# Kernel optimization log

Hardware: AMD Instinct MI355X
Metric: run time of the kernel (lower is better)

## Reference

```python
import jax, jax.numpy as jnp
import numpy as np

WS = 7          # window size
NH = 12         # attention heads
D_STATE = 64    # mamba d_state
HEADDIM = 64    # mamba headdim


def layernorm(x, w, b):
    mu = jnp.mean(x, axis=-1, keepdims=True)
    var = jnp.mean((x - mu) ** 2, axis=-1, keepdims=True)
    return (x - mu) * jax.lax.rsqrt(var + 1e-5) * w + b


def mamba2(x, W_in, conv_w, conv_b, dt_bias, A_log, D, mnorm_w, W_out):
    # Mamba2 (SSD) forward: in_proj -> causal depthwise conv+silu -> selective scan -> gated RMSNorm -> out_proj
    B, L, dm = x.shape
    nheads = dt_bias.shape[0]
    d_inner = nheads * HEADDIM
    zxbcdt = x @ W_in                                   # (B,L,2*d_inner+2*d_state+nheads)
    z = zxbcdt[..., :d_inner]
    xBC = zxbcdt[..., d_inner:2 * d_inner + 2 * D_STATE]
    dt = zxbcdt[..., -nheads:]
    conv_dim = xBC.shape[-1]
    pad = conv_w.shape[-1] - 1
    xBC_t = jnp.swapaxes(xBC, 1, 2)                     # (B, conv_dim, L)
    conv_out = jax.lax.conv_general_dilated(
        xBC_t, conv_w[:, None, :], window_strides=(1,), padding=[(pad, 0)],
        feature_group_count=conv_dim, dimension_numbers=('NCH', 'OIH', 'NCH'))
    xBC = jax.nn.silu(jnp.swapaxes(conv_out, 1, 2) + conv_b)
    xs = xBC[..., :d_inner]
    Bm = xBC[..., d_inner:d_inner + D_STATE]            # (B,L,n)
    Cm = xBC[..., d_inner + D_STATE:]                   # (B,L,n)
    dt = jax.nn.softplus(dt + dt_bias)                  # (B,L,h)
    A = -jnp.exp(A_log)                                 # (h,)
    dA = jnp.exp(dt * A)                                # (B,L,h)
    xh = xs.reshape(B, L, nheads, HEADDIM)              # (B,L,h,p)

    def step(h, inp):
        dA_t, dt_t, x_t, B_t, C_t = inp                 # (B,h),(B,h),(B,h,p),(B,n),(B,n)
        dBx = (dt_t[..., None] * x_t)[..., None] * B_t[:, None, None, :]
        h = h * dA_t[..., None, None] + dBx             # (B,h,p,n)
        y = jnp.einsum('bhpn,bn->bhp', h, C_t)
        return h, y

    sw = lambda a: jnp.swapaxes(a, 0, 1)                # time-major
    h0 = jnp.zeros((B, nheads, HEADDIM, D_STATE), x.dtype)
    _, ys = jax.lax.scan(step, h0, (sw(dA), sw(dt), sw(xh), sw(Bm), sw(Cm)))
    y = jnp.swapaxes(ys, 0, 1) + D[None, None, :, None] * xh   # (B,L,h,p)
    y = y.reshape(B, L, d_inner)
    g = y * jax.nn.silu(z)                              # gated RMSNorm (norm_before_gate=False)
    g = g * jax.lax.rsqrt(jnp.mean(g * g, axis=-1, keepdims=True) + 1e-5) * mnorm_w
    return g @ W_out


def gated_window_attention(xw, qkv_w, qkv_b, gate_w, gate_b, proj_w, proj_b):
    B_, N, C = xw.shape
    hd = C // NH
    qkv = (xw @ qkv_w + qkv_b).reshape(B_, N, 3, NH, hd).transpose(2, 0, 3, 1, 4)
    q, k, v = qkv[0] * (hd ** -0.5), qkv[1], qkv[2]     # (B_,h,N,d)
    attn = jax.nn.softmax(jnp.einsum('bhnd,bhmd->bhnm', q, k), axis=-1)
    xa = jnp.einsum('bhnm,bhmd->bhnd', attn, v).transpose(0, 2, 1, 3)  # (B_,N,h,d)
    gate = jax.nn.sigmoid(xw @ gate_w + gate_b)[..., None]             # (B_,N,h,1)
    xa = (xa * gate).reshape(B_, N, C)
    return xa @ proj_w + proj_b


def lgs_forward(x, norm1_w, norm1_b, W_in, conv_w, conv_b, dt_bias, A_log, D, mnorm_w, W_out,
                qkv_w, qkv_b, gate_w, gate_b, proj_w, proj_b, fusion_w, fusion_b,
                norm2_w, norm2_b, fc1_w, fc1_b, fc2_w, fc2_b, H, W):
    B, L, C = x.shape
    shortcut = x
    xn = layernorm(x, norm1_w, norm1_b)
    # Branch A: Mamba2 global scan
    x_mamba = mamba2(xn, W_in, conv_w, conv_b, dt_bias, A_log, D, mnorm_w, W_out)
    # Branch B: gated window attention (shift_size=0 -> no roll, no mask)
    x2d = xn.reshape(B, H, W, C)
    xw = x2d.reshape(B, H // WS, WS, W // WS, WS, C).transpose(0, 1, 3, 2, 4, 5).reshape(-1, WS * WS, C)
    aw = gated_window_attention(xw, qkv_w, qkv_b, gate_w, gate_b, proj_w, proj_b)
    x_attn = aw.reshape(B, H // WS, W // WS, WS, WS, C).transpose(0, 1, 3, 2, 4, 5).reshape(B, L, C)
    # Fuse branches with 1x1 conv (== linear on channel dim)
    x_cat = jnp.concatenate([x_mamba, x_attn], axis=-1)   # (B,L,2C)
    x_fused = x_cat @ fusion_w + fusion_b
    x = shortcut + x_fused
    xn2 = layernorm(x, norm2_w, norm2_b)
    mlp = jax.nn.gelu(xn2 @ fc1_w + fc1_b, approximate=False) @ fc2_w + fc2_b
    return x + mlp


def setup_inputs() -> dict:
    key = jax.random.key(0)
    ks = jax.random.split(key, 16)
    B, H, W, C = 8, 56, 56, 384
    L = H * W
    d_inner, d_state, nheads_m, d_conv = 768, 64, 12, 4
    d_in_proj = 2 * d_inner + 2 * d_state + nheads_m   # 1676
    conv_dim = d_inner + 2 * d_state                   # 896
    s = 0.02
    return {
        'x': jax.random.normal(ks[0], (B, L, C), jnp.float32),
        'norm1_w': jnp.ones((C,), jnp.float32),
        'norm1_b': jnp.zeros((C,), jnp.float32),
        'W_in': jax.random.normal(ks[1], (C, d_in_proj), jnp.float32) * s,
        'conv_w': jax.random.normal(ks[2], (conv_dim, d_conv), jnp.float32) * 0.1,
        'conv_b': jnp.zeros((conv_dim,), jnp.float32),
        'dt_bias': jax.random.normal(ks[3], (nheads_m,), jnp.float32) * 0.5,
        'A_log': jnp.log(jax.random.uniform(ks[4], (nheads_m,), jnp.float32, 1.0, 16.0)),
        'D': jnp.ones((nheads_m,), jnp.float32),
        'mnorm_w': jnp.ones((d_inner,), jnp.float32),
        'W_out': jax.random.normal(ks[5], (d_inner, C), jnp.float32) * s,
        'qkv_w': jax.random.normal(ks[6], (C, 3 * C), jnp.float32) * s,
        'qkv_b': jnp.zeros((3 * C,), jnp.float32),
        'gate_w': jax.random.normal(ks[7], (C, NH), jnp.float32) * s,
        'gate_b': jnp.zeros((NH,), jnp.float32),
        'proj_w': jax.random.normal(ks[8], (C, C), jnp.float32) * s,
        'proj_b': jnp.zeros((C,), jnp.float32),
        'fusion_w': jax.random.normal(ks[9], (2 * C, C), jnp.float32) * s,
        'fusion_b': jnp.zeros((C,), jnp.float32),
        'norm2_w': jnp.ones((C,), jnp.float32),
        'norm2_b': jnp.zeros((C,), jnp.float32),
        'fc1_w': jax.random.normal(ks[10], (C, 4 * C), jnp.float32) * s,
        'fc1_b': jnp.zeros((4 * C,), jnp.float32),
        'fc2_w': jax.random.normal(ks[11], (4 * C, C), jnp.float32) * s,
        'fc2_b': jnp.zeros((C,), jnp.float32),
        'H': H,
        'W': W,
    }


def reference(x, norm1_w, norm1_b, W_in, conv_w, conv_b, dt_bias, A_log, D, mnorm_w, W_out,
              qkv_w, qkv_b, gate_w, gate_b, proj_w, proj_b, fusion_w, fusion_b,
              norm2_w, norm2_b, fc1_w, fc1_b, fc2_w, fc2_b, H, W):
    return lgs_forward(x, norm1_w, norm1_b, W_in, conv_w, conv_b, dt_bias, A_log, D, mnorm_w, W_out,
                       qkv_w, qkv_b, gate_w, gate_b, proj_w, proj_b, fusion_w, fusion_b,
                       norm2_w, norm2_b, fc1_w, fc1_b, fc2_w, fc2_b, H, W)
```

## Files before the change

kernel.cpp:

```cpp
#include <hip/hip_runtime.h>
#include <math.h>

static constexpr int L_SEQ  = 3136;
static constexpr int NBATCH = 8;
static constexpr int CDIM   = 384;
static constexpr int DIN    = 768;
static constexpr int NHM    = 12;
static constexpr int HDM    = 64;
static constexpr int DPROJ  = 1676;
static constexpr int CONVD  = 896;
static constexpr int NROWS  = NBATCH * L_SEQ;
static constexpr int NHA    = 12;
static constexpr int NCH    = 49;
static constexpr int CHT    = 64;
static constexpr int CTK    = 28;

typedef __attribute__((ext_vector_type(8))) short short8;
typedef __attribute__((ext_vector_type(8))) unsigned short ushort8;
typedef __attribute__((ext_vector_type(4))) float f32x4;
typedef const unsigned int __attribute__((address_space(1)))* gua_t;
typedef unsigned int __attribute__((address_space(3)))* lua_t;

__device__ __forceinline__ float siluf(float x) { return x / (1.f + __expf(-x)); }
__device__ __forceinline__ unsigned short f2bf(float f) {
  unsigned int u = __float_as_uint(f);
  u += 0x7fff + ((u >> 16) & 1);
  return (unsigned short)(u >> 16);
}
__device__ __forceinline__ float bf2f(unsigned short h) {
  return __uint_as_float(((unsigned int)h) << 16);
}
__device__ __forceinline__ float fast_erff(float x) {
  float ax = fabsf(x);
  float tt = 1.f / (1.f + 0.3275911f * ax);
  float y = tt * (0.254829592f + tt * (-0.284496736f + tt * (1.421413741f +
            tt * (-1.453152027f + tt * 1.061405429f))));
  float r = 1.f - y * __expf(-ax * ax);
  return copysignf(r, x);
}

__global__ __launch_bounds__(256) void ln_kernel(const float* __restrict__ in,
    const float* __restrict__ w, const float* __restrict__ b, unsigned short* __restrict__ out) {
  int wave = threadIdx.x >> 6, lane = threadIdx.x & 63;
  int row = blockIdx.x * 4 + wave;
  if (row >= NROWS) return;
  const float* r = in + (size_t)row * CDIM;
  float2 v[3];
  float s1 = 0.f, s2 = 0.f;
#pragma unroll
  for (int q = 0; q < 3; q++) {
    v[q] = *(const float2*)&r[q * 128 + lane * 2];
    s1 += v[q].x + v[q].y;
    s2 += v[q].x * v[q].x + v[q].y * v[q].y;
  }
#pragma unroll
  for (int o = 32; o > 0; o >>= 1) { s1 += __shfl_xor(s1, o, 64); s2 += __shfl_xor(s2, o, 64); }
  float mu = s1 * (1.f / 384.f);
  float var = s2 * (1.f / 384.f) - mu * mu;
  float rs = rsqrtf(var + 1e-5f);
  unsigned short* o = out + (size_t)row * CDIM;
#pragma unroll
  for (int q = 0; q < 3; q++) {
    int c = q * 128 + lane * 2;
    float2 wv = *(const float2*)&w[c];
    float2 bv = *(const float2*)&b[c];
    float ox = (v[q].x - mu) * rs * wv.x + bv.x;
    float oy = (v[q].y - mu) * rs * wv.y + bv.y;
    unsigned int pk = (unsigned int)f2bf(ox) | ((unsigned int)f2bf(oy) << 16);
    *(unsigned int*)&o[c] = pk;
  }
}

__global__ __launch_bounds__(256) void wconv_kernel(const float* __restrict__ W,
    unsigned short* __restrict__ WT, int K, int N, int ldw) {
  __shared__ float tile[32][33];
  int k0 = blockIdx.x * 32, n0 = blockIdx.y * 32;
  int tx = threadIdx.x & 31, ty = threadIdx.x >> 5;
#pragma unroll
  for (int j = 0; j < 4; j++) {
    int k = k0 + ty + j * 8;
    int n = n0 + tx;
    tile[ty + j * 8][tx] = (n < N) ? W[(size_t)k * ldw + n] : 0.f;
  }
  __syncthreads();
#pragma unroll
  for (int j = 0; j < 4; j++) {
    int n = n0 + ty + j * 8;
    int k = k0 + tx;
    WT[(size_t)n * K + k] = f2bf(tile[tx][ty + j * 8]);
  }
}

template<int ACT, bool HASBIAS, bool HASRES, bool OUTBF>
__global__ __launch_bounds__(256) void gemm_bf(
    const unsigned short* __restrict__ A, const unsigned short* __restrict__ WT,
    void* __restrict__ Cp, const float* __restrict__ bias,
    const float* __restrict__ res, int ldr,
    int M, int N, int K, int lda, int ldc, int coff)
{
  __shared__ unsigned short As[3][128][32];
  __shared__ unsigned short Ws[3][128][32];
  int t = threadIdx.x;
  int gx = gridDim.x;
  int nwg = gx * gridDim.y;
  int orig = blockIdx.y * gx + blockIdx.x;
  int qq = nwg >> 3, rr = nwg & 7;
  int xcd = orig & 7, seq = orig >> 3;
  int wgid = (xcd < rr ? xcd * (qq + 1) : rr * (qq + 1) + (xcd - rr) * qq) + seq;
  int m0 = (wgid / gx) * 128, n0 = (wgid % gx) * 128;

  int lane = t & 63, w = t >> 6;
  int wr = (w >> 1) * 64, wc = (w & 1) * 64;
  int fl = lane & 15, kq = lane >> 4;
  int so = ((kq ^ ((lane >> 1) & 3))) * 8;
  f32x4 acc[4][4];
#pragma unroll
  for (int i = 0; i < 4; i++)
#pragma unroll
    for (int j = 0; j < 4; j++) acc[i][j] = (f32x4)0.f;

  auto stage = [&](int buf, int k0) {
#pragma unroll
    for (int j = 0; j < 2; j++) {
      int c = j * 256 + t;
      int row = c >> 2, qs = c & 3;
      int qsrc = qs ^ ((row >> 1) & 3);
      __builtin_amdgcn_global_load_lds(
          (gua_t)&A[(size_t)(m0 + row) * lda + k0 + qsrc * 8],
          (lua_t)&As[buf][0][0] + (size_t)c * 4, 16, 0, 0);
      __builtin_amdgcn_global_load_lds(
          (gua_t)&WT[(size_t)(n0 + row) * K + k0 + qsrc * 8],
          (lua_t)&Ws[buf][0][0] + (size_t)c * 4, 16, 0, 0);
    }
  };

  int nk = K >> 5;
  stage(0, 0);
  int sb = 1, rb = 0;
  for (int ks = 0; ks < nk; ks++) {
    if (ks + 1 < nk) {
      stage(sb, (ks + 1) << 5);
      sb = sb == 2 ? 0 : sb + 1;
      asm volatile("s_waitcnt vmcnt(4)" ::: "memory");
    } else {
      asm volatile("s_waitcnt vmcnt(0)" ::: "memory");
    }
    __builtin_amdgcn_s_barrier();
    asm volatile("" ::: "memory");
    __builtin_amdgcn_sched_barrier(0);
    short8 af[4], bfr[4];
#pragma unroll
    for (int mi = 0; mi < 4; mi++) af[mi] = *(const short8*)&As[rb][wr + mi * 16 + fl][so];
#pragma unroll
    for (int ni = 0; ni < 4; ni++) bfr[ni] = *(const short8*)&Ws[rb][wc + ni * 16 + fl][so];
    rb = rb == 2 ? 0 : rb + 1;
#pragma unroll
    for (int mi = 0; mi < 4; mi++)
#pragma unroll
      for (int ni = 0; ni < 4; ni++)
        acc[mi][ni] = __builtin_amdgcn_mfma_f32_16x16x32_bf16(af[mi], bfr[ni], acc[mi][ni], 0, 0, 0);
  }
  int rbase = (lane >> 4) * 4, cl = lane & 15;
#pragma unroll
  for (int mi = 0; mi < 4; mi++) {
#pragma unroll
    for (int ni = 0; ni < 4; ni++) {
      int n = n0 + wc + ni * 16 + cl;
      if (n >= N) continue;
#pragma unroll
      for (int r = 0; r < 4; r++) {
        int m = m0 + wr + mi * 16 + rbase + r;
        float v = acc[mi][ni][r];
        if (HASBIAS) v += bias[n];
        if (ACT == 1) v = 0.5f * v * (1.f + fast_erff(v * 0.70710678118654752f));
        if (HASRES) v += res[(size_t)m * ldr + n];
        if (OUTBF) ((unsigned short*)Cp)[(size_t)m * ldc + coff + n] = f2bf(v);
        else       ((float*)Cp)[(size_t)m * ldc + coff + n] = v;
      }
    }
  }
}

__global__ void dtprep_kernel(float* __restrict__ DT, const float* __restrict__ dt_bias,
    const float* __restrict__ A_log, float* __restrict__ DA) {
  int idx = blockIdx.x * blockDim.x + threadIdx.x;
  if (idx >= NROWS * NHM) return;
  int h = idx % NHM;
  float v = DT[idx] + dt_bias[h];
  float sp = (v > 20.f) ? v : log1pf(expf(v));
  DT[idx] = sp;
  DA[idx] = -expf(A_log[h]) * sp;
}

__global__ __launch_bounds__(256) void conv_bf_kernel(const unsigned short* __restrict__ xbc,
    const float* __restrict__ cw, const float* __restrict__ cb, unsigned short* __restrict__ XC) {
  int t = blockIdx.x * 256 + threadIdx.x;
  int c8 = t % 112;
  int rg = t / 112;
  int b = rg / 112, lc = rg % 112;
  int l0 = lc * CTK;
  int c0 = c8 * 8;
  float w0[8], w1[8], w2[8], w3[8], bq[8];
#pragma unroll
  for (int i = 0; i < 8; i++) {
    bq[i] = cb[c0 + i];
    float4 w4 = *(const float4*)&cw[(c0 + i) * 4];
    w0[i] = w4.x; w1[i] = w4.y; w2[i] = w4.z; w3[i] = w4.w;
  }
  const unsigned short* base = xbc + (size_t)b * L_SEQ * CONVD + c0;
  unsigned short* obase = XC + (size_t)b * L_SEQ * CONVD + c0;
  ushort8 h0 = (ushort8)0, h1 = (ushort8)0, h2 = (ushort8)0;
  if (l0 >= 3) {
    h0 = *(const ushort8*)&base[(size_t)(l0 - 3) * CONVD];
    h1 = *(const ushort8*)&base[(size_t)(l0 - 2) * CONVD];
    h2 = *(const ushort8*)&base[(size_t)(l0 - 1) * CONVD];
  }
  for (int i = 0; i < CTK; i++) {
    ushort8 cur = *(const ushort8*)&base[(size_t)(l0 + i) * CONVD];
    ushort8 ov;
#pragma unroll
    for (int q = 0; q < 8; q++) {
      float acc = bq[q] + w0[q] * bf2f(h0[q]) + w1[q] * bf2f(h1[q])
                + w2[q] * bf2f(h2[q]) + w3[q] * bf2f(cur[q]);
      ov[q] = f2bf(siluf(acc));
    }
    *(ushort8*)&obase[(size_t)(l0 + i) * CONVD] = ov;
    h0 = h1; h1 = h2; h2 = cur;
  }
}

__global__ __launch_bounds__(256) void mscan1_kernel(const unsigned short* __restrict__ XC,
    const float* __restrict__ dtp, const float* __restrict__ dta,
    float* __restrict__ H, float* __restrict__ QS) {
  __shared__ unsigned short Xt[64 * 72];
  __shared__ unsigned short Bt[64 * 72];
  __shared__ float lcs[64];
  __shared__ float wss[64];
  int ch = blockIdx.x, bh = blockIdx.y;
  int b = bh / NHM, head = bh - b * NHM;
  int t = threadIdx.x;
  int l0 = ch * CHT;
  const unsigned short* xcb = XC + ((size_t)b * L_SEQ + l0) * CONVD;
  if (t < 64) {
    size_t ro = ((size_t)b * L_SEQ + l0 + t) * NHM + head;
    float s = dta[ro];
#pragma unroll
    for (int o = 1; o < 64; o <<= 1) {
      float u = __shfl_up(s, o, 64);
      if (t >= o) s += u;
    }
    float lc63 = __shfl(s, 63, 64);
    lcs[t] = s;
    wss[t] = dtp[ro] * __expf(lc63 - s);
    if (t == 63) QS[bh * NCH + ch] = __expf(s);
  }
  __syncthreads();
#pragma unroll
  for (int it = 0; it < 16; it++) {
    int e = it * 256 + t;
    int j = e >> 6, cc = e & 63;
    const unsigned short* rowp = xcb + (size_t)j * CONVD;
    Xt[cc * 72 + j] = rowp[head * HDM + cc];
    Bt[cc * 72 + j] = f2bf(bf2f(rowp[768 + cc]) * wss[j]);
  }
  __syncthreads();
  int lane = t & 63, w = t >> 6;
  int wr = (w >> 1) * 32, wc = (w & 1) * 32;
  int fl = lane & 15, kq = lane >> 4;
  f32x4 acc[2][2];
#pragma unroll
  for (int i = 0; i < 2; i++)
#pragma unroll
    for (int j = 0; j < 2; j++) acc[i][j] = (f32x4)0.f;
#pragma unroll
  for (int kk = 0; kk < 2; kk++) {
    short8 af[2], bfr[2];
#pragma unroll
    for (int mi = 0; mi < 2; mi++)
      af[mi] = *(const short8*)&Xt[(wr + mi * 16 + fl) * 72 + kk * 32 + kq * 8];
#pragma unroll
    for (int ni = 0; ni < 2; ni++)
      bfr[ni] = *(const short8*)&Bt[(wc + ni * 16 + fl) * 72 + kk * 32 + kq * 8];
#pragma unroll
    for (int mi = 0; mi < 2; mi++)
#pragma unroll
      for (int ni = 0; ni < 2; ni++)
        acc[mi][ni] = __builtin_amdgcn_mfma_f32_16x16x32_bf16(af[mi], bfr[ni], acc[mi][ni], 0, 0, 0);
  }
  float* Hp = H + ((size_t)bh * NCH + ch) * 4096;
  int rbase = kq * 4, cl = fl;
#pragma unroll
  for (int mi = 0; mi < 2; mi++)
#pragma unroll
    for (int ni = 0; ni < 2; ni++)
#pragma unroll
      for (int r = 0; r < 4; r++)
        Hp[(size_t)(wr + mi * 16 + rbase + r) * 64 + wc + ni * 16 + cl] = acc[mi][ni][r];
}

__global__ __launch_bounds__(64) void scomb_kernel(float* __restrict__ H,
    const float* __restrict__ QS) {
  int bh = blockIdx.x;
  int e = (blockIdx.y * 64 + threadIdx.x) * 4;
  float4 cur = make_float4(0.f, 0.f, 0.f, 0.f);
  for (int s = 0; s < NCH; s++) {
    float* Hp = H + ((size_t)bh * NCH + s) * 4096 + e;
    float q = QS[bh * NCH + s];
    float4 tmp = *(float4*)Hp;
    *(float4*)Hp = cur;
    cur.x = q * cur.x + tmp.x;
    cur.y = q * cur.y + tmp.y;
    cur.z = q * cur.z + tmp.z;
    cur.w = q * cur.w + tmp.w;
  }
}

__global__ __launch_bounds__(256) void mscan2_kernel(const unsigned short* __restrict__ XC,
    const float* __restrict__ dtp, const float* __restrict__ dta,
    const float* __restrict__ H, const float* __restrict__ Dp,
    unsigned short* __restrict__ Ybf) {
  __shared__ unsigned short Cs[64 * 72];
  __shared__ unsigned short Bs[64 * 72];
  __shared__ unsigned short Xt[64 * 72];
  __shared__ unsigned short Hs[64 * 72];
  __shared__ unsigned short Ss[64 * 72];
  __shared__ float lcs[64];
  __shared__ float dts[64];
  int ch = blockIdx.x, bh = blockIdx.y;
  int b = bh / NHM, head = bh - b * NHM;
  int t = threadIdx.x;
  int l0 = ch * CHT;
  const unsigned short* xcb = XC + ((size_t)b * L_SEQ + l0) * CONVD;
  const float* Hg = H + ((size_t)bh * NCH + ch) * 4096;
  if (t < 64) {
    size_t ro = ((size_t)b * L_SEQ + l0 + t) * NHM + head;
    float s = dta[ro];
#pragma unroll
    for (int o = 1; o < 64; o <<= 1) {
      float u = __shfl_up(s, o, 64);
      if (t >= o) s += u;
    }
    lcs[t] = s;
    dts[t] = dtp[ro];
  }
#pragma unroll
  for (int it = 0; it < 16; it++) {
    int e = it * 256 + t;
    int j = e >> 6, cc = e & 63;
    const unsigned short* rowp = xcb + (size_t)j * CONVD;
    Xt[cc * 72 + j] = rowp[head * HDM + cc];
    Bs[j * 72 + cc] = rowp[768 + cc];
    Cs[j * 72 + cc] = rowp[832 + cc];
    Hs[j * 72 + cc] = f2bf(Hg[e]);
  }
  __syncthreads();
  int lane = t & 63, w = t >> 6;
  int wr = (w >> 1) * 32, wc = (w & 1) * 32;
  int fl = lane & 15, kq = lane >> 4;
  int rbase = kq * 4, cl = fl;
  f32x4 sacc[2][2];
#pragma unroll
  for (int i = 0; i < 2; i++)
#pragma unroll
    for (int j = 0; j < 2; j++) sacc[i][j] = (f32x4)0.f;
#pragma unroll
  for (int kk = 0; kk < 2; kk++) {
    short8 af[2], bfr[2];
#pragma unroll
    for (int mi = 0; mi < 2; mi++)
      af[mi] = *(const short8*)&Cs[(wr + mi * 16 + fl) * 72 + kk * 32 + kq * 8];
#pragma unroll
    for (int ni = 0; ni < 2; ni++)
      bfr[ni] = *(const short8*)&Bs[(wc + ni * 16 + fl) * 72 + kk * 32 + kq * 8];
#pragma unroll
    for (int mi = 0; mi < 2; mi++)
#pragma unroll
      for (int ni = 0; ni < 2; ni++)
        sacc[mi][ni] = __builtin_amdgcn_mfma_f32_16x16x32_bf16(af[mi], bfr[ni], sacc[mi][ni], 0, 0, 0);
  }
  __syncthreads();
#pragma unroll
  for (int mi = 0; mi < 2; mi++)
#pragma unroll
    for (int ni = 0; ni < 2; ni++)
#pragma unroll
      for (int r = 0; r < 4; r++) {
        int i = wr + mi * 16 + rbase + r;
        int j = wc + ni * 16 + cl;
        float v = (j <= i) ? sacc[mi][ni][r] * dts[j] * __expf(lcs[i] - lcs[j]) : 0.f;
        Ss[i * 72 + j] = f2bf(v);
      }
#pragma unroll
  for (int it = 0; it < 16; it++) {
    int e = it * 256 + t;
    int i = e >> 6, n = e & 63;
    float cv = bf2f(Cs[i * 72 + n]) * __expf(lcs[i]);
    Cs[i * 72 + n] = f2bf(cv);
  }
  __syncthreads();
  f32x4 yacc[2][2];
#pragma unroll
  for (int i = 0; i < 2; i++)
#pragma unroll
    for (int j = 0; j < 2; j++) yacc[i][j] = (f32x4)0.f;
#pragma unroll
  for (int kk = 0; kk < 2; kk++) {
    short8 af[2], bfr[2];
#pragma unroll
    for (int mi = 0; mi < 2; mi++)
      af[mi] = *(const short8*)&Ss[(wr + mi * 16 + fl) * 72 + kk * 32 + kq * 8];
#pragma unroll
    for (int ni = 0; ni < 2; ni++)
      bfr[ni] = *(const short8*)&Xt[(wc + ni * 16 + fl) * 72 + kk * 32 + kq * 8];
#pragma unroll
    for (int mi = 0; mi < 2; mi++)
#pragma unroll
      for (int ni = 0; ni < 2; ni++)
        yacc[mi][ni] = __builtin_amdgcn_mfma_f32_16x16x32_bf16(af[mi], bfr[ni], yacc[mi][ni], 0, 0, 0);
  }
#pragma unroll
  for (int kk = 0; kk < 2; kk++) {
    short8 af[2], bfr[2];
#pragma unroll
    for (int mi = 0; mi < 2; mi++)
      af[mi] = *(const short8*)&Cs[(wr + mi * 16 + fl) * 72 + kk * 32 + kq * 8];
#pragma unroll
    for (int ni = 0; ni < 2; ni++)
      bfr[ni] = *(const short8*)&Hs[(wc + ni * 16 + fl) * 72 + kk * 32 + kq * 8];
#pragma unroll
    for (int mi = 0; mi < 2; mi++)
#pragma unroll
      for (int ni = 0; ni < 2; ni++)
        yacc[mi][ni] = __builtin_amdgcn_mfma_f32_16x16x32_bf16(af[mi], bfr[ni], yacc[mi][ni], 0, 0, 0);
  }
  float Dh = Dp[head];
  unsigned short* yb = Ybf + ((size_t)b * L_SEQ + l0) * DIN + head * HDM;
#pragma unroll
  for (int mi = 0; mi < 2; mi++)
#pragma unroll
    for (int ni = 0; ni < 2; ni++)
#pragma unroll
      for (int r = 0; r < 4; r++) {
        int i = wr + mi * 16 + rbase + r;
        int p = wc + ni * 16 + cl;
        float xval = bf2f(Xt[p * 72 + i]);
        yb[(size_t)i * DIN + p] = f2bf(yacc[mi][ni][r] + Dh * xval);
      }
}

__global__ __launch_bounds__(256) void gate_rms_kernel(unsigned short* __restrict__ Y,
    const unsigned short* __restrict__ Z, const float* __restrict__ mw) {
  int wave = threadIdx.x >> 6, lane = threadIdx.x & 63;
  int row = blockIdx.x * 4 + wave;
  if (row >= NROWS) return;
  unsigned short* y = Y + (size_t)row * DIN;
  const unsigned short* z = Z + (size_t)row * DIN;
  float g[12];
  float ss = 0.f;
#pragma unroll
  for (int q = 0; q < 3; q++) {
    int c = q * 256 + lane * 4;
    uint2 yu = *(const uint2*)&y[c];
    uint2 zu = *(const uint2*)&z[c];
    float y0 = bf2f((unsigned short)(yu.x & 0xffff));
    float y1 = bf2f((unsigned short)(yu.x >> 16));
    float y2 = bf2f((unsigned short)(yu.y & 0xffff));
    float y3 = bf2f((unsigned short)(yu.y >> 16));
    float z0 = bf2f((unsigned short)(zu.x & 0xffff));
    float z1 = bf2f((unsigned short)(zu.x >> 16));
    float z2 = bf2f((unsigned short)(zu.y & 0xffff));
    float z3 = bf2f((unsigned short)(zu.y >> 16));
    float g0 = y0 * siluf(z0), g1 = y1 * siluf(z1);
    float g2 = y2 * siluf(z2), g3 = y3 * siluf(z3);
    ss += g0 * g0 + g1 * g1 + g2 * g2 + g3 * g3;
    g[q * 4 + 0] = g0; g[q * 4 + 1] = g1; g[q * 4 + 2] = g2; g[q * 4 + 3] = g3;
  }
#pragma unroll
  for (int o = 32; o > 0; o >>= 1) ss += __shfl_xor(ss, o, 64);
  float rs = rsqrtf(ss * (1.f / 768.f) + 1e-5f);
#pragma unroll
  for (int q = 0; q < 3; q++) {
    int c = q * 256 + lane * 4;
    float4 m = *(const float4*)&mw[c];
    unsigned int lo = (unsigned int)f2bf(g[q*4+0] * rs * m.x) | ((unsigned int)f2bf(g[q*4+1] * rs * m.y) << 16);
    unsigned int hi = (unsigned int)f2bf(g[q*4+2] * rs * m.z) | ((unsigned int)f2bf(g[q*4+3] * rs * m.w) << 16);
    uint2 pk; pk.x = lo; pk.y = hi;
    *(uint2*)&y[c] = pk;
  }
}

__global__ __launch_bounds__(256) void attgate_kernel(const unsigned short* __restrict__ XN,
    const float* __restrict__ gw, const float* __restrict__ gb, float* __restrict__ G) {
  int wave = threadIdx.x >> 6, lane = threadIdx.x & 63;
  int row = blockIdx.x * 4 + wave;
  if (row >= NROWS) return;
  const unsigned short* x = XN + (size_t)row * CDIM;
  float acc[12] = {};
#pragma unroll
  for (int q = 0; q < 6; q++) {
    int k = q * 64 + lane;
    float xv = bf2f(x[k]);
    const float* wr = gw + (size_t)k * 12;
    float4 w0 = *(const float4*)&wr[0];
    float4 w1 = *(const float4*)&wr[4];
    float4 w2 = *(const float4*)&wr[8];
    acc[0] += xv * w0.x; acc[1] += xv * w0.y; acc[2]  += xv * w0.z; acc[3]  += xv * w0.w;
    acc[4] += xv * w1.x; acc[5] += xv * w1.y; acc[6]  += xv * w1.z; acc[7]  += xv * w1.w;
    acc[8] += xv * w2.x; acc[9] += xv * w2.y; acc[10] += xv * w2.z; acc[11] += xv * w2.w;
  }
#pragma unroll
  for (int h = 0; h < 12; h++)
#pragma unroll
    for (int o = 32; o > 0; o >>= 1) acc[h] += __shfl_xor(acc[h], o, 64);
  if (lane == 0) {
#pragma unroll
    for (int h = 0; h < 12; h++) {
      float v = acc[h] + gb[h];
      G[(size_t)row * 12 + h] = 1.f / (1.f + expf(-v));
    }
  }
}

__global__ __launch_bounds__(256) void attn_kernel(const unsigned short* __restrict__ QKV,
    const float* __restrict__ G, unsigned short* __restrict__ XA) {
  __shared__ float qs[49 * 33];
  __shared__ float kst[32 * 52];
  __shared__ float vs[49 * 32];
  __shared__ float ps[49 * 52];
  int blk = blockIdx.x;
  int head = blk % NHA;
  int win = blk / NHA;
  int b = win >> 6;
  int wr = win & 63;
  int wy = wr >> 3, wx = wr & 7;
  int t = threadIdx.x;
  const float scale = 0.17677669529663688f;

  for (int e = t; e < 1568; e += 256) {
    int tok = e >> 5, d = e & 31;
    int iy = tok / 7, ix = tok - iy * 7;
    size_t rl = (size_t)b * L_SEQ + (wy * 7 + iy) * 56 + (wx * 7 + ix);
    const unsigned short* qp = QKV + rl * 1152 + head * 32 + d;
    qs[tok * 33 + d] = bf2f(qp[0]) * scale;
    kst[d * 52 + tok] = bf2f(qp[384]);
    vs[tok * 32 + d] = bf2f(qp[768]);
  }
  if (t < 96) kst[(t & 31) * 52 + 49 + (t >> 5)] = 0.f;
  __syncthreads();

  for (int e = t; e < 637; e += 256) {
    int qi = e / 13, g = e - qi * 13;
    const float* qrow = &qs[qi * 33];
    float4 acc = make_float4(0.f, 0.f, 0.f, 0.f);
#pragma unroll
    for (int dd = 0; dd < 32; dd++) {
      float qv = qrow[dd];
      float4 kv = *(const float4*)&kst[dd * 52 + g * 4];
      acc.x += qv * kv.x; acc.y += qv * kv.y;
      acc.z += qv * kv.z; acc.w += qv * kv.w;
    }
    *(float4*)&ps[qi * 52 + g * 4] = acc;
  }
  __syncthreads();
  if (t < 49) {
    float* pr = &ps[t * 52];
    float m = pr[0];
    for (int j = 1; j < 49; j++) m = fmaxf(m, pr[j]);
    float s = 0.f;
    for (int j = 0; j < 49; j++) { float e2 = expf(pr[j] - m); pr[j] = e2; s += e2; }
    float inv = 1.f / s;
    for (int j = 0; j < 49; j++) pr[j] *= inv;
  }
  __syncthreads();
  for (int e = t; e < 1568; e += 256) {
    int qi = e >> 5, d = e & 31;
    const float* pr = &ps[qi * 52];
    float acc = 0.f;
    for (int j = 0; j < 49; j++) acc += pr[j] * vs[j * 32 + d];
    int iy = qi / 7, ix = qi - iy * 7;
    size_t rg = (size_t)b * L_SEQ + (wy * 7 + iy) * 56 + (wx * 7 + ix);
    float g = G[rg * 12 + head];
    XA[rg * CDIM + head * 32 + d] = f2bf(acc * g);
  }
}

extern "C" void kernel_launch(void* const* d_in, const int* in_sizes, int n_in,
                              void* d_out, int out_size, void* d_ws, size_t ws_size,
                              hipStream_t stream) {
  const float* x        = (const float*)d_in[0];
  const float* norm1_w  = (const float*)d_in[1];
  const float* norm1_b  = (const float*)d_in[2];
  const float* W_in     = (const float*)d_in[3];
  const float* conv_w   = (const float*)d_in[4];
  const float* conv_b   = (const float*)d_in[5];
  const float* dt_bias  = (const float*)d_in[6];
  const float* A_log    = (const float*)d_in[7];
  const float* Dp       = (const float*)d_in[8];
  const float* mnorm_w  = (const float*)d_in[9];
  const float* W_out    = (const float*)d_in[10];
  const float* qkv_w    = (const float*)d_in[11];
  const float* qkv_b    = (const float*)d_in[12];
  const float* gate_w   = (const float*)d_in[13];
  const float* gate_b   = (const float*)d_in[14];
  const float* proj_w   = (const float*)d_in[15];
  const float* proj_b   = (const float*)d_in[16];
  const float* fusion_w = (const float*)d_in[17];
  const float* fusion_b = (const float*)d_in[18];
  const float* norm2_w  = (const float*)d_in[19];
  const float* norm2_b  = (const float*)d_in[20];
  const float* fc1_w    = (const float*)d_in[21];
  const float* fc1_b    = (const float*)d_in[22];
  const float* fc2_w    = (const float*)d_in[23];
  const float* fc2_b    = (const float*)d_in[24];
  float* OUT = (float*)d_out;

  float* ws = (float*)d_ws;
  unsigned short* XNBF = (unsigned short*)ws;
  float* XC_  = ws + 4816896;
  float* SCR  = XC_ + 22478848;
  unsigned short* YBF = (unsigned short*)(SCR + 22478848);
  unsigned short* WT  = (unsigned short*)(SCR + 22478848 + 9633792);
  float* DT_ = (float*)(WT + 3047424);
  float* DA_ = DT_ + 301056;
  float* G_  = DA_ + 301056;
  float* QS_ = G_  + 301056;

  unsigned short* XBCBF = (unsigned short*)SCR;
  unsigned short* XCBF  = (unsigned short*)XC_;
  float* H_ = SCR;
  unsigned short* ZBF   = (unsigned short*)SCR;
  unsigned short* QKVBF = (unsigned short*)SCR;
  unsigned short* M1BF  = (unsigned short*)SCR;
  unsigned short* CATBF = (unsigned short*)XC_;
  unsigned short* XABF  = (unsigned short*)(XC_ + 9633792);

  unsigned short* wt_xbc  = WT;
  unsigned short* wt_dt   = WT + 344064;
  unsigned short* wt_z    = WT + 393216;
  unsigned short* wt_out  = WT + 688128;
  unsigned short* wt_qkv  = WT + 983040;
  unsigned short* wt_proj = WT + 1425408;
  unsigned short* wt_fus  = WT + 1572864;
  unsigned short* wt_fc1  = WT + 1867776;
  unsigned short* wt_fc2  = WT + 2457600;

  wconv_kernel<<<dim3(12,  28), 256, 0, stream>>>(W_in + 768,  wt_xbc,  384,  896, DPROJ);
  wconv_kernel<<<dim3(12,   4), 256, 0, stream>>>(W_in + 1664, wt_dt,   384,   12, DPROJ);
  wconv_kernel<<<dim3(12,  24), 256, 0, stream>>>(W_in,        wt_z,    384,  768, DPROJ);
  wconv_kernel<<<dim3(24,  12), 256, 0, stream>>>(W_out,       wt_out,  768,  384, 384);
  wconv_kernel<<<dim3(12,  36), 256, 0, stream>>>(qkv_w,       wt_qkv,  384, 1152, 1152);
  wconv_kernel<<<dim3(12,  12), 256, 0, stream>>>(proj_w,      wt_proj, 384,  384, 384);
  wconv_kernel<<<dim3(24,  12), 256, 0, stream>>>(fusion_w,    wt_fus,  768,  384, 384);
  wconv_kernel<<<dim3(12,  48), 256, 0, stream>>>(fc1_w,       wt_fc1,  384, 1536, 1536);
  wconv_kernel<<<dim3(48,  12), 256, 0, stream>>>(fc2_w,       wt_fc2, 1536,  384, 384);

  ln_kernel<<<6272, 256, 0, stream>>>(x, norm1_w, norm1_b, XNBF);

  gemm_bf<0, false, false, true><<<dim3(7, 196), 256, 0, stream>>>(
      XNBF, wt_xbc, XBCBF, nullptr, nullptr, 0, NROWS, CONVD, CDIM, CDIM, CONVD, 0);
  conv_bf_kernel<<<392, 256, 0, stream>>>(XBCBF, conv_w, conv_b, XCBF);
  gemm_bf<0, false, false, false><<<dim3(1, 196), 256, 0, stream>>>(
      XNBF, wt_dt, DT_, nullptr, nullptr, 0, NROWS, NHM, CDIM, CDIM, NHM, 0);

  dtprep_kernel<<<(NROWS * NHM + 255) / 256, 256, 0, stream>>>(DT_, dt_bias, A_log, DA_);

  mscan1_kernel<<<dim3(NCH, 96), 256, 0, stream>>>(XCBF, DT_, DA_, H_, QS_);
  scomb_kernel<<<dim3(96, 16), 64, 0, stream>>>(H_, QS_);
  mscan2_kernel<<<dim3(NCH, 96), 256, 0, stream>>>(XCBF, DT_, DA_, H_, Dp, YBF);

  gemm_bf<0, false, false, true><<<dim3(6, 196), 256, 0, stream>>>(
      XNBF, wt_z, ZBF, nullptr, nullptr, 0, NROWS, DIN, CDIM, CDIM, DIN, 0);
  gate_rms_kernel<<<6272, 256, 0, stream>>>(YBF, ZBF, mnorm_w);

  gemm_bf<0, false, false, true><<<dim3(3, 196), 256, 0, stream>>>(
      YBF, wt_out, CATBF, nullptr, nullptr, 0, NROWS, CDIM, DIN, DIN, 2 * CDIM, 0);

  attgate_kernel<<<6272, 256, 0, stream>>>(XNBF, gate_w, gate_b, G_);

  gemm_bf<0, true, false, true><<<dim3(9, 196), 256, 0, stream>>>(
      XNBF, wt_qkv, QKVBF, qkv_b, nullptr, 0, NROWS, 3 * CDIM, CDIM, CDIM, 3 * CDIM, 0);
  attn_kernel<<<512 * NHA, 256, 0, stream>>>(QKVBF, G_, XABF);

  gemm_bf<0, true, false, true><<<dim3(3, 196), 256, 0, stream>>>(
      XABF, wt_proj, CATBF, proj_b, nullptr, 0, NROWS, CDIM, CDIM, CDIM, 2 * CDIM, CDIM);

  gemm_bf<0, true, true, false><<<dim3(3, 196), 256, 0, stream>>>(
      CATBF, wt_fus, OUT, fusion_b, x, CDIM, NROWS, CDIM, 2 * CDIM, 2 * CDIM, CDIM, 0);

  ln_kernel<<<6272, 256, 0, stream>>>(OUT, norm2_w, norm2_b, XNBF);

  gemm_bf<1, true, false, true><<<dim3(12, 196), 256, 0, stream>>>(
      XNBF, wt_fc1, M1BF, fc1_b, nullptr, 0, NROWS, 4 * CDIM, CDIM, CDIM, 4 * CDIM, 0);
  gemm_bf<0, true, true, false><<<dim3(3, 196), 256, 0, stream>>>(
      M1BF, wt_fc2, OUT, fc2_b, OUT, CDIM, NROWS, CDIM, 4 * CDIM, 4 * CDIM, CDIM, 0);
}
```

Measured before the change: 742.1 us.

## Rewrite window attention with single-wave bf16 MFMA and in-register softmax

Replaces the scalar fp32 shared-memory window attention with a single 64-lane wave per (window, head). QK^T and PV now run on 16x16x32 bf16 MFMA instructions, with Q/K loaded straight into registers and softmax done in registers using cross-lane shuffles. Only the probabilities and a swizzled transposed V go through LDS, which removes most barriers and LDS traffic. In exchange, probabilities are rounded to bf16 and the kernel pads 49 tokens up to 64.

```diff
diff --git a/kernel.cpp b/kernel.cpp
--- a/kernel.cpp
+++ b/kernel.cpp
@@ -521,66 +521,123 @@
   }
 }
 
-__global__ __launch_bounds__(256) void attn_kernel(const unsigned short* __restrict__ QKV,
+__global__ __launch_bounds__(64) void attn_kernel(const unsigned short* __restrict__ QKV,
     const float* __restrict__ G, unsigned short* __restrict__ XA) {
-  __shared__ float qs[49 * 33];
-  __shared__ float kst[32 * 52];
-  __shared__ float vs[49 * 32];
-  __shared__ float ps[49 * 52];
+  __shared__ unsigned short Pl[64 * 72];
+  __shared__ unsigned short Vt[32 * 72];
   int blk = blockIdx.x;
   int head = blk % NHA;
   int win = blk / NHA;
   int b = win >> 6;
-  int wr = win & 63;
-  int wy = wr >> 3, wx = wr & 7;
-  int t = threadIdx.x;
+  int wrw = win & 63;
+  int wy = wrw >> 3, wx = wrw & 7;
+  int lane = threadIdx.x;
+  int fl = lane & 15, kq = lane >> 4;
   const float scale = 0.17677669529663688f;
-
-  for (int e = t; e < 1568; e += 256) {
-    int tok = e >> 5, d = e & 31;
+  size_t bbase = (size_t)b * L_SEQ;
+  const unsigned short* qb = QKV + head * 32;
+
+  short8 aq[4], bk[4];
+#pragma unroll
+  for (int ti = 0; ti < 4; ti++) {
+    int tok = ti * 16 + fl; if (tok > 48) tok = 48;
     int iy = tok / 7, ix = tok - iy * 7;
-    size_t rl = (size_t)b * L_SEQ + (wy * 7 + iy) * 56 + (wx * 7 + ix);
-    const unsigned short* qp = QKV + rl * 1152 + head * 32 + d;
-    qs[tok * 33 + d] = bf2f(qp[0]) * scale;
-    kst[d * 52 + tok] = bf2f(qp[384]);
-    vs[tok * 32 + d] = bf2f(qp[768]);
-  }
-  if (t < 96) kst[(t & 31) * 52 + 49 + (t >> 5)] = 0.f;
-  __syncthreads();
-
-  for (int e = t; e < 637; e += 256) {
-    int qi = e / 13, g = e - qi * 13;
-    const float* qrow = &qs[qi * 33];
-    float4 acc = make_float4(0.f, 0.f, 0.f, 0.f);
-#pragma unroll
-    for (int dd = 0; dd < 32; dd++) {
-      float qv = qrow[dd];
-      float4 kv = *(const float4*)&kst[dd * 52 + g * 4];
-      acc.x += qv * kv.x; acc.y += qv * kv.y;
-      acc.z += qv * kv.z; acc.w += qv * kv.w;
-    }
-    *(float4*)&ps[qi * 52 + g * 4] = acc;
-  }
-  __syncthreads();
-  if (t < 49) {
-    float* pr = &ps[t * 52];
-    float m = pr[0];
-    for (int j = 1; j < 49; j++) m = fmaxf(m, pr[j]);
-    float s = 0.f;
-    for (int j = 0; j < 49; j++) { float e2 = expf(pr[j] - m); pr[j] = e2; s += e2; }
-    float inv = 1.f / s;
-    for (int j = 0; j < 49; j++) pr[j] *= inv;
-  }
-  __syncthreads();
-  for (int e = t; e < 1568; e += 256) {
-    int qi = e >> 5, d = e & 31;
-    const float* pr = &ps[qi * 52];
-    float acc = 0.f;
-    for (int j = 0; j < 49; j++) acc += pr[j] * vs[j * 32 + d];
-    int iy = qi / 7, ix = qi - iy * 7;
-    size_t rg = (size_t)b * L_SEQ + (wy * 7 + iy) * 56 + (wx * 7 + ix);
-    float g = G[rg * 12 + head];
-    XA[rg * CDIM + head * 32 + d] = f2bf(acc * g);
+    size_t r = bbase + (size_t)(wy * 7 + iy) * 56 + wx * 7 + ix;
+    aq[ti] = *(const short8*)&qb[r * 1152 + kq * 8];
+    bk[ti] = *(const short8*)&qb[r * 1152 + 384 + kq * 8];
+  }
+#pragma unroll
+  for (int it = 0; it < 4; it++) {
+    int j = (lane >> 2) + it * 16;
+    int dc = (lane & 3) * 8;
+    ushort8 v8 = (ushort8)0;
+    if (j <= 48) {
+      int iy = j / 7, ix = j - iy * 7;
+      size_t r = bbase + (size_t)(wy * 7 + iy) * 56 + wx * 7 + ix;
+      v8 = *(const ushort8*)&qb[r * 1152 + 768 + dc];
+    }
+#pragma unroll
+    for (int q2 = 0; q2 < 8; q2++) {
+      int d = dc + q2;
+      Vt[d * 72 + (((j >> 3) ^ (d >> 3)) << 3) + (j & 7)] = v8[q2];
+    }
+  }
+  f32x4 sacc[4][4];
+#pragma unroll
+  for (int tj = 0; tj < 4; tj++)
+#pragma unroll
+    for (int ti = 0; ti < 4; ti++)
+      sacc[tj][ti] = __builtin_amdgcn_mfma_f32_16x16x32_bf16(bk[tj], aq[ti], (f32x4)0.f, 0, 0, 0);
+#pragma unroll
+  for (int ti = 0; ti < 4; ti++) {
+    float mx = -1e30f;
+#pragma unroll
+    for (int tj = 0; tj < 4; tj++)
+#pragma unroll
+      for (int r = 0; r < 4; r++) {
+        int j = tj * 16 + kq * 4 + r;
+        float v = (j < 49) ? sacc[tj][ti][r] * scale : -1e30f;
+        sacc[tj][ti][r] = v;
+        mx = fmaxf(mx, v);
+      }
+    mx = fmaxf(mx, __shfl_xor(mx, 16, 64));
+    mx = fmaxf(mx, __shfl_xor(mx, 32, 64));
+    float sum = 0.f;
+#pragma unroll
+    for (int tj = 0; tj < 4; tj++)
+#pragma unroll
+      for (int r = 0; r < 4; r++) {
+        float e = __expf(sacc[tj][ti][r] - mx);
+        sacc[tj][ti][r] = e;
+        sum += e;
+      }
+    sum += __shfl_xor(sum, 16, 64);
+    sum += __shfl_xor(sum, 32, 64);
+    float inv = 1.f / sum;
+    int i = ti * 16 + fl;
+#pragma unroll
+    for (int tj = 0; tj < 4; tj++)
+#pragma unroll
+      for (int r = 0; r < 4; r++) {
+        int j = tj * 16 + kq * 4 + r;
+        Pl[i * 72 + j] = f2bf(sacc[tj][ti][r] * inv);
+      }
+  }
+  f32x4 oacc[4][2];
+#pragma unroll
+  for (int i2 = 0; i2 < 4; i2++)
+#pragma unroll
+    for (int nd = 0; nd < 2; nd++) oacc[i2][nd] = (f32x4)0.f;
+#pragma unroll
+  for (int kk = 0; kk < 2; kk++) {
+    short8 ap[4], bv[2];
+#pragma unroll
+    for (int i2 = 0; i2 < 4; i2++)
+      ap[i2] = *(const short8*)&Pl[(i2 * 16 + fl) * 72 + kk * 32 + kq * 8];
+#pragma unroll
+    for (int nd = 0; nd < 2; nd++) {
+      int d = nd * 16 + fl;
+      bv[nd] = *(const short8*)&Vt[d * 72 + (((kk * 4 + kq) ^ (d >> 3)) << 3)];
+    }
+#pragma unroll
+    for (int i2 = 0; i2 < 4; i2++)
+#pragma unroll
+      for (int nd = 0; nd < 2; nd++)
+        oacc[i2][nd] = __builtin_amdgcn_mfma_f32_16x16x32_bf16(ap[i2], bv[nd], oacc[i2][nd], 0, 0, 0);
+  }
+#pragma unroll
+  for (int i2 = 0; i2 < 4; i2++) {
+#pragma unroll
+    for (int r = 0; r < 4; r++) {
+      int i = i2 * 16 + kq * 4 + r;
+      if (i > 48) continue;
+      int iy = i / 7, ix = i - iy * 7;
+      size_t rg = bbase + (size_t)(wy * 7 + iy) * 56 + wx * 7 + ix;
+      float g = G[rg * 12 + head];
+#pragma unroll
+      for (int nd = 0; nd < 2; nd++)
+        XA[rg * CDIM + head * 32 + nd * 16 + fl] = f2bf(oacc[i2][nd][r] * g);
+    }
   }
 }
 
@@ -679,7 +736,7 @@
 
   gemm_bf<0, true, false, true><<<dim3(9, 196), 256, 0, stream>>>(
       XNBF, wt_qkv, QKVBF, qkv_b, nullptr, 0, NROWS, 3 * CDIM, CDIM, CDIM, 3 * CDIM, 0);
-  attn_kernel<<<512 * NHA, 256, 0, stream>>>(QKVBF, G_, XABF);
+  attn_kernel<<<512 * NHA, 64, 0, stream>>>(QKVBF, G_, XABF);
 
   gemm_bf<0, true, false, true><<<dim3(3, 196), 256, 0, stream>>>(
       XABF, wt_proj, CATBF, proj_b, nullptr, 0, NROWS, CDIM, CDIM, CDIM, 2 * CDIM, CDIM);
```

Measured after the change: 698.4 us. 1.06x faster.
